# Kernel optimization log

Measured on AMD Instinct MI355X. Metric: run time of the kernel, lower is better.

## Reference

```python
import jax, jax.numpy as jnp
import numpy as np


def setup_inputs() -> dict:
    key = jax.random.key(0)
    k1, k2, k3 = jax.random.split(key, 3)
    B, L, D = 8, 4096, 320
    CB_DIM, N_BOOKS = 16, 8192
    input_values = jax.random.normal(k1, (B, L, D), dtype=jnp.float32)
    # mask all ones -> static masked-select shape N = B*L
    mask_time_indices = jnp.ones((B, L), dtype=jnp.int32)
    # xavier_uniform for Linear(D -> CB_DIM, bias=False): limit = sqrt(6/(fan_in+fan_out))
    limit = float(np.sqrt(6.0 / (D + CB_DIM)))
    proj_weight = jax.random.uniform(k2, (CB_DIM, D), dtype=jnp.float32, minval=-limit, maxval=limit)
    code_book = jax.random.normal(k3, (N_BOOKS, CB_DIM), dtype=jnp.float32)
    return {"input_values": input_values, "mask_time_indices": mask_time_indices,
            "proj_weight": proj_weight, "code_book": code_book}


def reference(input_values, mask_time_indices, proj_weight, code_book):
    # input_values: [B, L, D]; mask is all-ones so masked select == flatten (static shape N=B*L)
    B, L, D = input_values.shape
    flat = input_values.reshape(B * L, D)  # [N, D]
    targets = flat @ proj_weight.T  # [N, cb_dim]  (random projection, no bias)
    # argmin over Euclidean norm == argmin over squared distance (monotone),
    # expanded form avoids the [N, n_books, cb_dim] broadcast intermediate.
    t2 = jnp.sum(targets * targets, axis=-1, keepdims=True)        # [N, 1]
    c2 = jnp.sum(code_book * code_book, axis=-1)                   # [n_books]
    d2 = t2 - 2.0 * (targets @ code_book.T) + c2                   # [N, n_books]
    labels = jnp.argmin(d2, axis=-1)                               # [N]
    return labels
```

## Files before the change

kernel.cpp:

```cpp
#include <hip/hip_runtime.h>

#define N_ROWS 32768
#define D_IN 320
#define CB 16
#define N_BOOKS 8192

typedef __attribute__((ext_vector_type(8))) short bf16x8;
typedef __attribute__((ext_vector_type(4))) float f32x4;
#define MFMA __builtin_amdgcn_mfma_f32_16x16x32_bf16

__device__ __forceinline__ unsigned short bf16rn(float f) {
  unsigned u = __float_as_uint(f);
  u += 0x7fffu + ((u >> 16) & 1u);
  return (unsigned short)(u >> 16);
}
__device__ __forceinline__ float bf16tof(unsigned short h) {
  return __uint_as_float(((unsigned)h) << 16);
}

__global__ __launch_bounds__(256) void prep_kernel(const float* __restrict__ cbk,
                                                   short* __restrict__ bfrag,
                                                   float* __restrict__ nh_g) {
  const int j = blockIdx.x * 256 + threadIdx.x;
  const float4* src = (const float4*)(cbk + (size_t)j * CB);
  float4 a = src[0], b = src[1], c = src[2], d = src[3];
  float ce[16] = {a.x, a.y, a.z, a.w, b.x, b.y, b.z, b.w,
                  c.x, c.y, c.z, c.w, d.x, d.y, d.z, d.w};
  short c1[16], c2[16], c3[16];
  double s = 0.0;
#pragma unroll
  for (int i = 0; i < 16; i++) {
    s += (double)ce[i] * (double)ce[i];
    unsigned short x1 = bf16rn(ce[i]);
    float r1 = ce[i] - bf16tof(x1);
    unsigned short x2 = bf16rn(r1);
    float r2 = r1 - bf16tof(x2);
    unsigned short x3 = bf16rn(r2);
    c1[i] = (short)x1; c2[i] = (short)x2; c3[i] = (short)x3;
  }
  nh_g[j] = (float)(-0.5 * s);
  bf16x8 lo1, hi1, lo2, hi2, lo3, hi3;
#pragma unroll
  for (int i = 0; i < 8; i++) {
    lo1[i] = c1[i]; hi1[i] = c1[i + 8];
    lo2[i] = c2[i]; hi2[i] = c2[i + 8];
    lo3[i] = c3[i]; hi3[i] = c3[i + 8];
  }
  const int bt = j >> 4, n = j & 15;
  short* base = bfrag + (size_t)bt * 1536;
  *(bf16x8*)(base + 0 * 512 + (0 * 16 + n) * 8) = lo1;
  *(bf16x8*)(base + 0 * 512 + (1 * 16 + n) * 8) = hi1;
  *(bf16x8*)(base + 0 * 512 + (2 * 16 + n) * 8) = lo1;
  *(bf16x8*)(base + 0 * 512 + (3 * 16 + n) * 8) = hi1;
  *(bf16x8*)(base + 1 * 512 + (0 * 16 + n) * 8) = lo2;
  *(bf16x8*)(base + 1 * 512 + (1 * 16 + n) * 8) = hi2;
  *(bf16x8*)(base + 1 * 512 + (2 * 16 + n) * 8) = lo2;
  *(bf16x8*)(base + 1 * 512 + (3 * 16 + n) * 8) = hi2;
  *(bf16x8*)(base + 2 * 512 + (0 * 16 + n) * 8) = lo3;
  *(bf16x8*)(base + 2 * 512 + (1 * 16 + n) * 8) = hi3;
  *(bf16x8*)(base + 2 * 512 + (2 * 16 + n) * 8) = lo1;
  *(bf16x8*)(base + 2 * 512 + (3 * 16 + n) * 8) = hi1;
}

__global__ __launch_bounds__(256, 2) void proj_kernel(const float* __restrict__ x,
                                                      const float* __restrict__ w,
                                                      short* __restrict__ tsplit) {
  __shared__ __align__(16) short wfrag[3][10][64][8];
  __shared__ __align__(16) float xs[2][64 * 36];
  const int tid = threadIdx.x;
  const int lane = tid & 63;
  const int wv = tid >> 6;

  for (int i = tid; i < D_IN * CB; i += 256) {
    int d = i >> 4, o = i & 15;
    float f = w[o * D_IN + d];
    unsigned short h1 = bf16rn(f);
    float r1 = f - bf16tof(h1);
    unsigned short h2 = bf16rn(r1);
    float r2 = r1 - bf16tof(h2);
    unsigned short h3 = bf16rn(r2);
    int c = d >> 5, qq = (d >> 3) & 3, pos = d & 7;
    int ln = qq * 16 + o;
    wfrag[0][c][ln][pos] = (short)h1;
    wfrag[1][c][ln][pos] = (short)h2;
    wfrag[2][c][ln][pos] = (short)h3;
  }

  const float* xblk = x + (size_t)blockIdx.x * 64 * D_IN;
  {
    int row = tid >> 2, k0 = (tid & 3) * 8;
    float4 v0 = *(const float4*)(xblk + row * D_IN + k0);
    float4 v1 = *(const float4*)(xblk + row * D_IN + k0 + 4);
    *(float4*)&xs[0][row * 36 + k0] = v0;
    *(float4*)&xs[0][row * 36 + k0 + 4] = v1;
  }
  __syncthreads();

  const int m = lane & 15, q = lane >> 4;
  double dacc[4] = {0.0, 0.0, 0.0, 0.0};
  for (int c = 0; c < 10; c++) {
    const int buf = c & 1;
    if (c < 9) {
      int row = tid >> 2, k0 = (tid & 3) * 8;
      float4 v0 = *(const float4*)(xblk + row * D_IN + (c + 1) * 32 + k0);
      float4 v1 = *(const float4*)(xblk + row * D_IN + (c + 1) * 32 + k0 + 4);
      *(float4*)&xs[buf ^ 1][row * 36 + k0] = v0;
      *(float4*)&xs[buf ^ 1][row * 36 + k0 + 4] = v1;
    }
    const float* xp = &xs[buf][(wv * 16 + m) * 36 + q * 8];
    float4 xa = *(const float4*)xp;
    float4 xb = *(const float4*)(xp + 4);
    float xe[8] = {xa.x, xa.y, xa.z, xa.w, xb.x, xb.y, xb.z, xb.w};
    bf16x8 a1, a2, a3;
#pragma unroll
    for (int j = 0; j < 8; j++) {
      unsigned short h1 = bf16rn(xe[j]);
      float r1 = xe[j] - bf16tof(h1);
      unsigned short h2 = bf16rn(r1);
      float r2 = r1 - bf16tof(h2);
      unsigned short h3 = bf16rn(r2);
      a1[j] = (short)h1; a2[j] = (short)h2; a3[j] = (short)h3;
    }
    bf16x8 b1 = *(const bf16x8*)wfrag[0][c][lane];
    bf16x8 b2 = *(const bf16x8*)wfrag[1][c][lane];
    bf16x8 b3 = *(const bf16x8*)wfrag[2][c][lane];
    f32x4 g = {0.f, 0.f, 0.f, 0.f};
    g = MFMA(a1, b1, g, 0, 0, 0);
#pragma unroll
    for (int r = 0; r < 4; r++) dacc[r] += (double)g[r];
    g = (f32x4){0.f, 0.f, 0.f, 0.f};
    g = MFMA(a2, b1, g, 0, 0, 0);
    g = MFMA(a1, b2, g, 0, 0, 0);
#pragma unroll
    for (int r = 0; r < 4; r++) dacc[r] += (double)g[r];
    g = (f32x4){0.f, 0.f, 0.f, 0.f};
    g = MFMA(a3, b1, g, 0, 0, 0);
    g = MFMA(a1, b3, g, 0, 0, 0);
    g = MFMA(a2, b2, g, 0, 0, 0);
#pragma unroll
    for (int r = 0; r < 4; r++) dacc[r] += (double)g[r];
    __syncthreads();
  }

  float* tl = (float*)xs;
#pragma unroll
  for (int r = 0; r < 4; r++) tl[(wv * 16 + q * 4 + r) * 17 + m] = (float)dacc[r];
  __syncthreads();
  {
    int row_l = tid >> 2, p = tid & 3;
    short h1[4], h2[4], h3[4];
#pragma unroll
    for (int i = 0; i < 4; i++) {
      float f = tl[row_l * 17 + p * 4 + i];
      unsigned short a = bf16rn(f);
      float r1 = f - bf16tof(a);
      unsigned short b = bf16rn(r1);
      float r2 = r1 - bf16tof(b);
      unsigned short cc = bf16rn(r2);
      h1[i] = (short)a; h2[i] = (short)b; h3[i] = (short)cc;
    }
    size_t base = (size_t)(blockIdx.x * 64 + row_l) * 48;
    *(short4*)(tsplit + base + p * 4) = make_short4(h1[0], h1[1], h1[2], h1[3]);
    *(short4*)(tsplit + base + 16 + p * 4) = make_short4(h2[0], h2[1], h2[2], h2[3]);
    *(short4*)(tsplit + base + 32 + p * 4) = make_short4(h3[0], h3[1], h3[2], h3[3]);
  }
}

#define SC_H 8

__global__ __attribute__((amdgpu_flat_work_group_size(256, 256)))
__attribute__((amdgpu_waves_per_eu(2, 4)))
void score_kernel(const short* __restrict__ tsplit,
                  const short* __restrict__ bfrag,
                  const float* __restrict__ nh_g,
                  float4* __restrict__ cand) {
  const int tid = threadIdx.x;
  const int lane = tid & 63;
  const int wv = tid >> 6;
  const int m = lane & 15, q = lane >> 4;
  const int rb = blockIdx.x & 127;
  const int h = blockIdx.x >> 7;
  const int rowbase = rb * 256;

  bf16x8 A12[4], A13[4];
#pragma unroll
  for (int rt = 0; rt < 4; rt++) {
    int row = rowbase + wv * 64 + rt * 16 + m;
    const short* tp = tsplit + (size_t)row * 48;
    A12[rt] = *(const bf16x8*)(tp + q * 8);
    A13[rt] = *(const bf16x8*)(tp + q * 8 + ((q >= 2) ? 16 : 0));
  }

  float s1[4][4], s2[4][4];
  int i1[4][4];
#pragma unroll
  for (int rt = 0; rt < 4; rt++)
#pragma unroll
    for (int r = 0; r < 4; r++) { s1[rt][r] = -3.4e38f; s2[rt][r] = -3.4e38f; i1[rt][r] = 0; }

  const short* gq = bfrag + (size_t)h * 98304 + lane * 8;
  const float* nhp = nh_g + h * 1024 + m;

  bf16x8 b1 = *(const bf16x8*)(gq);
  bf16x8 b2 = *(const bf16x8*)(gq + 512);
  bf16x8 b3 = *(const bf16x8*)(gq + 1024);
  float nh0 = nhp[0];

  for (int bt = 0; bt < 64; bt++) {
    const short* bp = gq + (bt + 1) * 1536;
    bf16x8 n1 = *(const bf16x8*)(bp);
    bf16x8 n2 = *(const bf16x8*)(bp + 512);
    bf16x8 n3 = *(const bf16x8*)(bp + 1024);
    float nn = nhp[(bt + 1) * 16];

    f32x4 ci = {nh0, nh0, nh0, nh0};
    const int colv = h * 1024 + bt * 16 + m;
#pragma unroll
    for (int rt = 0; rt < 4; rt++) {
      f32x4 acc = MFMA(A12[rt], b1, ci, 0, 0, 0);
      acc = MFMA(A12[rt], b2, acc, 0, 0, 0);
      acc = MFMA(A13[rt], b3, acc, 0, 0, 0);
#pragma unroll
      for (int r = 0; r < 4; r++) {
        float v = acc[r];
        float s1o = s1[rt][r];
        s2[rt][r] = __builtin_amdgcn_fmed3f(v, s1o, s2[rt][r]);
        s1[rt][r] = fmaxf(s1o, v);
        i1[rt][r] = (v > s1o) ? colv : i1[rt][r];
      }
    }
    b1 = n1; b2 = n2; b3 = n3; nh0 = nn;
  }

#pragma unroll
  for (int rt = 0; rt < 4; rt++)
#pragma unroll
    for (int r = 0; r < 4; r++) {
      float a1v = s1[rt][r], a2v = s2[rt][r];
      int ai = i1[rt][r];
#pragma unroll
      for (int msk = 1; msk <= 8; msk <<= 1) {
        float o1 = __shfl_xor(a1v, msk);
        float o2 = __shfl_xor(a2v, msk);
        int oi = __shfl_xor(ai, msk);
        if (o1 > a1v) {
          a2v = fmaxf(a1v, o2); a1v = o1; ai = oi;
        } else {
          a2v = fmaxf(a2v, o1);
          if (o1 == a1v && oi < ai) ai = oi;
        }
      }
      if (m == 0) {
        int row = rowbase + wv * 64 + rt * 16 + q * 4 + r;
        cand[(size_t)h * N_ROWS + row] = make_float4(a1v, a2v, __int_as_float(ai), 0.f);
      }
    }
}

#define MARGIN_EPS 1.0e-4f

__global__ __launch_bounds__(256) void reduce_fb_kernel(const float4* __restrict__ cand,
                                                        const float* __restrict__ x,
                                                        const float* __restrict__ w,
                                                        const float* __restrict__ codebook,
                                                        int* __restrict__ out) {
  __shared__ int flagged[256];
  __shared__ double ps[16][17];
  __shared__ double tsh[16];
  __shared__ double rs[256];
  __shared__ int ri[256];
  const int tid = threadIdx.x;
  const int base = blockIdx.x * 256;
  {
    const int r = base + tid;
    float S1 = -3.4e38f, S2 = -3.4e38f;
    int I = 0;
#pragma unroll
    for (int h = 0; h < SC_H; h++) {
      float4 v = cand[(size_t)h * N_ROWS + r];
      if (v.x > S1) {
        S2 = fmaxf(S1, v.y); S1 = v.x; I = __float_as_int(v.z);
      } else {
        S2 = fmaxf(S2, v.x);
      }
    }
    out[r] = I;
    flagged[tid] = (S1 - S2 < MARGIN_EPS) ? 1 : 0;
  }
  __syncthreads();

  for (int rr = 0; rr < 256; rr++) {
    if (!flagged[rr]) continue;
    const int row = base + rr;
    {
      int o = tid & 15, c = tid >> 4;
      double p = 0.0;
      for (int k = 0; k < 20; k++) {
        int d = c * 20 + k;
        p = fma((double)x[(size_t)row * D_IN + d], (double)w[o * D_IN + d], p);
      }
      ps[c][o] = p;
    }
    __syncthreads();
    if (tid < 16) {
      double t = 0.0;
      for (int c = 0; c < 16; c++) t += ps[c][tid];
      tsh[tid] = t;
    }
    __syncthreads();
    double t[16];
#pragma unroll
    for (int i = 0; i < 16; i++) t[i] = tsh[i];
    double bs = -1.0e300;
    int bi = 0;
    for (int j = tid; j < N_BOOKS; j += 256) {
      const float* cp = codebook + (size_t)j * CB;
      double dot = 0.0, cc = 0.0;
#pragma unroll
      for (int i = 0; i < 16; i++) {
        double cv = (double)cp[i];
        dot = fma(t[i], cv, dot);
        cc = fma(cv, cv, cc);
      }
      double mv = dot - 0.5 * cc;
      if (mv > bs) { bs = mv; bi = j; }
    }
    rs[tid] = bs; ri[tid] = bi;
    __syncthreads();
    for (int s = 128; s > 0; s >>= 1) {
      if (tid < s) {
        double os = rs[tid + s]; int oi = ri[tid + s];
        if (os > rs[tid] || (os == rs[tid] && oi < ri[tid])) { rs[tid] = os; ri[tid] = oi; }
      }
      __syncthreads();
    }
    if (tid == 0) out[row] = ri[0];
    __syncthreads();
  }
}

extern "C" void kernel_launch(void* const* d_in, const int* in_sizes, int n_in,
                              void* d_out, int out_size, void* d_ws, size_t ws_size,
                              hipStream_t stream) {
  (void)in_sizes; (void)n_in; (void)out_size; (void)ws_size;
  const float* x = (const float*)d_in[0];
  const float* w = (const float*)d_in[2];
  const float* codebook = (const float*)d_in[3];

  char* ws = (char*)d_ws;
  short* tsplit = (short*)(ws);
  short* bfrag = (short*)(ws + (3 << 20));
  float* nh_g = (float*)(ws + 4718592);
  float4* cand = (float4*)(ws + (5 << 20));
  int* out = (int*)d_out;

  prep_kernel<<<N_BOOKS / 256, 256, 0, stream>>>(codebook, bfrag, nh_g);
  proj_kernel<<<N_ROWS / 64, 256, 0, stream>>>(x, w, tsplit);
  score_kernel<<<128 * SC_H, 256, 0, stream>>>(tsplit, bfrag, nh_g, cand);
  reduce_fb_kernel<<<N_ROWS / 256, 256, 0, stream>>>(cand, x, w, codebook, out);
}
```

Measured before the change: 210.9 us.

## Compact flagged rows into global list and rescore with grid-stride kernel; serialize row tiles in scorer

The merge step now appends rows with a small top-2 margin to a global list through an atomic counter, and a separate grid-stride kernel recomputes only those rows in double precision. Before, each block looped over its own flagged rows, so a few blocks could carry most of the fallback work. The score kernel also runs its four row tiles one after another instead of holding all of them in registers at once. That lowers register pressure, but each tile re-streams the codebook fragments, which multiplies the B-operand loads by four.

```diff
diff --git a/kernel.cpp b/kernel.cpp
--- a/kernel.cpp
+++ b/kernel.cpp
@@ -20,7 +20,9 @@
 
 __global__ __launch_bounds__(256) void prep_kernel(const float* __restrict__ cbk,
                                                    short* __restrict__ bfrag,
-                                                   float* __restrict__ nh_g) {
+                                                   float* __restrict__ nh_g,
+                                                   int* __restrict__ ctr) {
+  if (blockIdx.x == 0 && threadIdx.x == 0) *ctr = 0;
   const int j = blockIdx.x * 256 + threadIdx.x;
   const float4* src = (const float4*)(cbk + (size_t)j * CB);
   float4 a = src[0], b = src[1], c = src[2], d = src[3];
@@ -168,12 +170,10 @@
 
 #define SC_H 8
 
-__global__ __attribute__((amdgpu_flat_work_group_size(256, 256)))
-__attribute__((amdgpu_waves_per_eu(2, 4)))
-void score_kernel(const short* __restrict__ tsplit,
-                  const short* __restrict__ bfrag,
-                  const float* __restrict__ nh_g,
-                  float4* __restrict__ cand) {
+__global__ __launch_bounds__(256, 2) void score_kernel(const short* __restrict__ tsplit,
+                                                       const short* __restrict__ bfrag,
+                                                       const float* __restrict__ nh_g,
+                                                       float4* __restrict__ cand) {
   const int tid = threadIdx.x;
   const int lane = tid & 63;
   const int wv = tid >> 6;
@@ -182,62 +182,54 @@
   const int h = blockIdx.x >> 7;
   const int rowbase = rb * 256;
 
-  bf16x8 A12[4], A13[4];
-#pragma unroll
+  const short* gq0 = bfrag + (size_t)h * 98304 + lane * 8;
+  const float* nhp = nh_g + h * 1024 + m;
+
+#pragma unroll 1
   for (int rt = 0; rt < 4; rt++) {
-    int row = rowbase + wv * 64 + rt * 16 + m;
-    const short* tp = tsplit + (size_t)row * 48;
-    A12[rt] = *(const bf16x8*)(tp + q * 8);
-    A13[rt] = *(const bf16x8*)(tp + q * 8 + ((q >= 2) ? 16 : 0));
-  }
-
-  float s1[4][4], s2[4][4];
-  int i1[4][4];
-#pragma unroll
-  for (int rt = 0; rt < 4; rt++)
-#pragma unroll
-    for (int r = 0; r < 4; r++) { s1[rt][r] = -3.4e38f; s2[rt][r] = -3.4e38f; i1[rt][r] = 0; }
-
-  const short* gq = bfrag + (size_t)h * 98304 + lane * 8;
-  const float* nhp = nh_g + h * 1024 + m;
-
-  bf16x8 b1 = *(const bf16x8*)(gq);
-  bf16x8 b2 = *(const bf16x8*)(gq + 512);
-  bf16x8 b3 = *(const bf16x8*)(gq + 1024);
-  float nh0 = nhp[0];
-
-  for (int bt = 0; bt < 64; bt++) {
-    const short* bp = gq + (bt + 1) * 1536;
-    bf16x8 n1 = *(const bf16x8*)(bp);
-    bf16x8 n2 = *(const bf16x8*)(bp + 512);
-    bf16x8 n3 = *(const bf16x8*)(bp + 1024);
-    float nn = nhp[(bt + 1) * 16];
-
-    f32x4 ci = {nh0, nh0, nh0, nh0};
-    const int colv = h * 1024 + bt * 16 + m;
-#pragma unroll
-    for (int rt = 0; rt < 4; rt++) {
-      f32x4 acc = MFMA(A12[rt], b1, ci, 0, 0, 0);
-      acc = MFMA(A12[rt], b2, acc, 0, 0, 0);
-      acc = MFMA(A13[rt], b3, acc, 0, 0, 0);
+    const int row0 = rowbase + wv * 64 + rt * 16 + m;
+    const short* tp = tsplit + (size_t)row0 * 48;
+    const bf16x8 A12 = *(const bf16x8*)(tp + q * 8);
+    const bf16x8 A13 = *(const bf16x8*)(tp + q * 8 + ((q >= 2) ? 16 : 0));
+
+    float s1[4], s2[4];
+    int i1[4];
+#pragma unroll
+    for (int r = 0; r < 4; r++) { s1[r] = -3.4e38f; s2[r] = -3.4e38f; i1[r] = 0; }
+
+    bf16x8 b1 = *(const bf16x8*)(gq0);
+    bf16x8 b2 = *(const bf16x8*)(gq0 + 512);
+    bf16x8 b3 = *(const bf16x8*)(gq0 + 1024);
+    float nh0 = nhp[0];
+    int colv = h * 1024 + m;
+
+    for (int bt = 0; bt < 64; bt++) {
+      const short* bp = gq0 + (bt + 1) * 1536;
+      bf16x8 n1 = *(const bf16x8*)(bp);
+      bf16x8 n2 = *(const bf16x8*)(bp + 512);
+      bf16x8 n3 = *(const bf16x8*)(bp + 1024);
+      float nn = nhp[(bt + 1) * 16];
+
+      f32x4 ci = {nh0, nh0, nh0, nh0};
+      f32x4 acc = MFMA(A12, b1, ci, 0, 0, 0);
+      acc = MFMA(A12, b2, acc, 0, 0, 0);
+      acc = MFMA(A13, b3, acc, 0, 0, 0);
 #pragma unroll
       for (int r = 0; r < 4; r++) {
         float v = acc[r];
-        float s1o = s1[rt][r];
-        s2[rt][r] = __builtin_amdgcn_fmed3f(v, s1o, s2[rt][r]);
-        s1[rt][r] = fmaxf(s1o, v);
-        i1[rt][r] = (v > s1o) ? colv : i1[rt][r];
-      }
-    }
-    b1 = n1; b2 = n2; b3 = n3; nh0 = nn;
-  }
-
-#pragma unroll
-  for (int rt = 0; rt < 4; rt++)
+        float s1o = s1[r];
+        s2[r] = __builtin_amdgcn_fmed3f(v, s1o, s2[r]);
+        s1[r] = fmaxf(s1o, v);
+        i1[r] = (v > s1o) ? colv : i1[r];
+      }
+      colv += 16;
+      b1 = n1; b2 = n2; b3 = n3; nh0 = nn;
+    }
+
 #pragma unroll
     for (int r = 0; r < 4; r++) {
-      float a1v = s1[rt][r], a2v = s2[rt][r];
-      int ai = i1[rt][r];
+      float a1v = s1[r], a2v = s2[r];
+      int ai = i1[r];
 #pragma unroll
       for (int msk = 1; msk <= 8; msk <<= 1) {
         float o1 = __shfl_xor(a1v, msk);
@@ -255,43 +247,49 @@
         cand[(size_t)h * N_ROWS + row] = make_float4(a1v, a2v, __int_as_float(ai), 0.f);
       }
     }
+  }
 }
 
 #define MARGIN_EPS 1.0e-4f
 
-__global__ __launch_bounds__(256) void reduce_fb_kernel(const float4* __restrict__ cand,
-                                                        const float* __restrict__ x,
-                                                        const float* __restrict__ w,
-                                                        const float* __restrict__ codebook,
-                                                        int* __restrict__ out) {
-  __shared__ int flagged[256];
+__global__ __launch_bounds__(256) void merge_flag_kernel(const float4* __restrict__ cand,
+                                                         int* __restrict__ out,
+                                                         int* __restrict__ list,
+                                                         int* __restrict__ ctr) {
+  const int r = blockIdx.x * 256 + threadIdx.x;
+  float S1 = -3.4e38f, S2 = -3.4e38f;
+  int I = 0;
+#pragma unroll
+  for (int h = 0; h < SC_H; h++) {
+    float4 v = cand[(size_t)h * N_ROWS + r];
+    if (v.x > S1) {
+      S2 = fmaxf(S1, v.y); S1 = v.x; I = __float_as_int(v.z);
+    } else {
+      S2 = fmaxf(S2, v.x);
+    }
+  }
+  out[r] = I;
+  if (S1 - S2 < MARGIN_EPS) {
+    int slot = atomicAdd(ctr, 1);
+    list[slot] = r;
+  }
+}
+
+__global__ __launch_bounds__(256) void rescore_kernel(const int* __restrict__ list,
+                                                      const int* __restrict__ ctr,
+                                                      const float* __restrict__ x,
+                                                      const float* __restrict__ w,
+                                                      const float* __restrict__ codebook,
+                                                      int* __restrict__ out) {
   __shared__ double ps[16][17];
   __shared__ double tsh[16];
   __shared__ double rs[256];
   __shared__ int ri[256];
   const int tid = threadIdx.x;
-  const int base = blockIdx.x * 256;
-  {
-    const int r = base + tid;
-    float S1 = -3.4e38f, S2 = -3.4e38f;
-    int I = 0;
-#pragma unroll
-    for (int h = 0; h < SC_H; h++) {
-      float4 v = cand[(size_t)h * N_ROWS + r];
-      if (v.x > S1) {
-        S2 = fmaxf(S1, v.y); S1 = v.x; I = __float_as_int(v.z);
-      } else {
-        S2 = fmaxf(S2, v.x);
-      }
-    }
-    out[r] = I;
-    flagged[tid] = (S1 - S2 < MARGIN_EPS) ? 1 : 0;
-  }
-  __syncthreads();
-
-  for (int rr = 0; rr < 256; rr++) {
-    if (!flagged[rr]) continue;
-    const int row = base + rr;
+  const int total = ctr[0];
+
+  for (int it = blockIdx.x; it < total; it += gridDim.x) {
+    const int row = list[it];
     {
       int o = tid & 15, c = tid >> 4;
       double p = 0.0;
@@ -351,11 +349,14 @@
   short* tsplit = (short*)(ws);
   short* bfrag = (short*)(ws + (3 << 20));
   float* nh_g = (float*)(ws + 4718592);
+  int* list = (int*)(ws + 4755456);
+  int* ctr = (int*)(ws + 4886528);
   float4* cand = (float4*)(ws + (5 << 20));
   int* out = (int*)d_out;
 
-  prep_kernel<<<N_BOOKS / 256, 256, 0, stream>>>(codebook, bfrag, nh_g);
+  prep_kernel<<<N_BOOKS / 256, 256, 0, stream>>>(codebook, bfrag, nh_g, ctr);
   proj_kernel<<<N_ROWS / 64, 256, 0, stream>>>(x, w, tsplit);
   score_kernel<<<128 * SC_H, 256, 0, stream>>>(tsplit, bfrag, nh_g, cand);
-  reduce_fb_kernel<<<N_ROWS / 256, 256, 0, stream>>>(cand, x, w, codebook, out);
-}
+  merge_flag_kernel<<<N_ROWS / 256, 256, 0, stream>>>(cand, out, list, ctr);
+  rescore_kernel<<<512, 256, 0, stream>>>(list, ctr, x, w, codebook, out);
+}
```

Result: slower. 226.0 us (+7.1%).
